# Kernel optimization log

Hardware: AMD Instinct MI355X
Metric: run time of the kernel (lower is better)

The kernel has to match this reference:

```python
import jax, jax.numpy as jnp
import numpy as np
import math

B = 16
IMG_H = IMG_W = 1024.0
FEAT_SIZES = [256, 128, 64, 32, 16]
A = 3
NUMS = [A * s * s for s in FEAT_SIZES]   # anchors per FPN level
TOTAL = sum(NUMS)                        # 261888
PRE_NMS_TOP_N = 1000
POST_NMS_TOP_N = 1000
NMS_THRESH = 0.7
SCORE_THRESH = 0.0
MIN_SIZE = 1e-3
BBOX_XFORM_CLIP = math.log(1000.0 / 16.0)
LEVELS = jnp.asarray(np.concatenate([np.full(n, i, dtype=np.int64) for i, n in enumerate(NUMS)]))


def setup_inputs() -> dict:
    key = jax.random.key(0)
    k1, k2, k3 = jax.random.split(key, 3)
    objectness = jax.random.normal(k1, (B, TOTAL), dtype=jnp.float32)
    deltas = jax.random.normal(k2, (B, TOTAL, 4), dtype=jnp.float32) * 0.2
    u = jax.random.uniform(k3, (TOTAL, 4), dtype=jnp.float32)
    ctr = u[:, :2] * jnp.array([IMG_W, IMG_H], dtype=jnp.float32)
    wh = u[:, 2:] * 192.0 + 16.0
    anchors = jnp.concatenate([ctr - 0.5 * wh, ctr + 0.5 * wh], axis=-1)
    return {"objectness": objectness, "deltas": deltas, "anchors": anchors}


def _decode(deltas, anchors):
    # BoxCoder with weights (1,1,1,1); deltas [B,T,4], anchors [T,4] (broadcast)
    w = anchors[:, 2] - anchors[:, 0]
    h = anchors[:, 3] - anchors[:, 1]
    cx = anchors[:, 0] + 0.5 * w
    cy = anchors[:, 1] + 0.5 * h
    dx, dy = deltas[..., 0], deltas[..., 1]
    dw = jnp.minimum(deltas[..., 2], BBOX_XFORM_CLIP)
    dh = jnp.minimum(deltas[..., 3], BBOX_XFORM_CLIP)
    pcx = dx * w + cx
    pcy = dy * h + cy
    pw = jnp.exp(dw) * w
    ph = jnp.exp(dh) * h
    return jnp.stack([pcx - 0.5 * pw, pcy - 0.5 * ph, pcx + 0.5 * pw, pcy + 0.5 * ph], axis=-1)


def _iou_one_vs_all(box, boxes):
    lt = jnp.maximum(box[:2], boxes[:, :2])
    rb = jnp.minimum(box[2:], boxes[:, 2:])
    wh = jnp.clip(rb - lt, 0.0)
    inter = wh[:, 0] * wh[:, 1]
    a1 = (box[2] - box[0]) * (box[3] - box[1])
    a2 = (boxes[:, 2] - boxes[:, 0]) * (boxes[:, 3] - boxes[:, 1])
    return inter / (a1 + a2 - inter)


def _nms_image(boxes, scores, lvl):
    # clip_boxes_to_image
    x = jnp.clip(boxes[:, 0::2], 0.0, IMG_W)
    y = jnp.clip(boxes[:, 1::2], 0.0, IMG_H)
    boxes = jnp.stack([x[:, 0], y[:, 0], x[:, 1], y[:, 1]], axis=-1)
    # remove_small_boxes + score_thresh, expressed as masking (fixed shapes)
    ws = boxes[:, 2] - boxes[:, 0]
    hs = boxes[:, 3] - boxes[:, 1]
    valid = (ws >= MIN_SIZE) & (hs >= MIN_SIZE) & (scores >= SCORE_THRESH)
    s0 = jnp.where(valid, scores, -1.0)
    # batched_nms: offset boxes by level so cross-level boxes never overlap
    off = lvl.astype(boxes.dtype) * (jnp.max(boxes) + 1.0)
    boff = boxes + off[:, None]

    def step(s, _):
        j = jnp.argmax(s)
        sj = s[j]
        take = sj > 0.0  # sigmoid scores are in (0,1); -1 marks suppressed
        iou = _iou_one_vs_all(boff[j], boff)
        s = jnp.where(iou > NMS_THRESH, -1.0, s)
        s = s.at[j].set(-1.0)
        out_b = jnp.where(take, boxes[j], jnp.zeros(4, boxes.dtype))
        out_s = jnp.where(take, sj, jnp.zeros((), boxes.dtype))
        return s, (out_b, out_s)

    _, (ob, os) = jax.lax.scan(step, s0, None, length=POST_NMS_TOP_N)
    return ob, os  # [P,4], [P]


def reference(objectness, deltas, anchors):
    proposals = _decode(deltas, anchors)  # [B, TOTAL, 4]
    # per-level top-k (pre-NMS), offsets into the flat anchor axis
    idx_list, offset = [], 0
    for n in NUMS:
        k = min(PRE_NMS_TOP_N, n)
        _, idx = jax.lax.top_k(objectness[:, offset:offset + n], k)
        idx_list.append(idx + offset)
        offset += n
    top_idx = jnp.concatenate(idx_list, axis=1)  # [B, K], K = 4768
    scores = jax.nn.sigmoid(jnp.take_along_axis(objectness, top_idx, axis=1))
    boxes = jnp.take_along_axis(proposals, top_idx[..., None], axis=1)
    lvl = LEVELS[top_idx]
    ob, os = jax.vmap(_nms_image)(boxes, scores, lvl)  # [B,P,4], [B,P]
    return jnp.concatenate([ob, os[..., None]], axis=-1)  # [B, P, 5]
```

## Files before the change

kernel.cpp:

```cpp
#include <hip/hip_runtime.h>
#include <math.h>

#pragma clang fp contract(off)

#define NLVL 5
#define TOTALN 261888
#define NBATCH 16
#define CAP 1024
#define NPROB (NBATCH * NLVL)
#define POST_N 1000
#define NMS_TH 0.7f
#define MINSZ 1e-3f
#define IMGSZ 1024.0f
#define BBOX_CLIP 4.135166556742356f

#define M_TH 0x1.666667p-1

#define HBINS 2048
#define CCAP 4096
#define NBLK 65
#define LMS 17
#define NPAIR 136

__constant__ int c_loff[NLVL] = {0, 196608, 245760, 258048, 261120};
__constant__ int c_k[NLVL]    = {1000, 1000, 1000, 1000, 768};
__constant__ int c_nch[NLVL]  = {48, 12, 3, 1, 1};

__constant__ unsigned char c_pw[NPAIR] = {
    0, 1,1, 2,2,2, 3,3,3,3, 4,4,4,4,4, 5,5,5,5,5,5, 6,6,6,6,6,6,6,
    7,7,7,7,7,7,7,7, 8,8,8,8,8,8,8,8,8, 9,9,9,9,9,9,9,9,9,9,
    10,10,10,10,10,10,10,10,10,10,10, 11,11,11,11,11,11,11,11,11,11,11,11,
    12,12,12,12,12,12,12,12,12,12,12,12,12, 13,13,13,13,13,13,13,13,13,13,13,13,13,13,
    14,14,14,14,14,14,14,14,14,14,14,14,14,14,14,
    15,15,15,15,15,15,15,15,15,15,15,15,15,15,15,15};
__constant__ unsigned char c_pr[NPAIR] = {
    0, 0,1, 0,1,2, 0,1,2,3, 0,1,2,3,4, 0,1,2,3,4,5, 0,1,2,3,4,5,6,
    0,1,2,3,4,5,6,7, 0,1,2,3,4,5,6,7,8, 0,1,2,3,4,5,6,7,8,9,
    0,1,2,3,4,5,6,7,8,9,10, 0,1,2,3,4,5,6,7,8,9,10,11,
    0,1,2,3,4,5,6,7,8,9,10,11,12, 0,1,2,3,4,5,6,7,8,9,10,11,12,13,
    0,1,2,3,4,5,6,7,8,9,10,11,12,13,14,
    0,1,2,3,4,5,6,7,8,9,10,11,12,13,14,15};

__device__ __forceinline__ unsigned monokey(float f) {
    unsigned b = __float_as_uint(f);
    return (b & 0x80000000u) ? ~b : (b | 0x80000000u);
}

__device__ __forceinline__ void blk_span(int b, int& lvl, int& start, int& cnt) {
    if (b < 48)      { lvl = 0; start = b * 4096;                  cnt = 4096; }
    else if (b < 60) { lvl = 1; start = 196608 + (b - 48) * 4096;  cnt = 4096; }
    else if (b < 63) { lvl = 2; start = 245760 + (b - 60) * 4096;  cnt = 4096; }
    else if (b == 63){ lvl = 3; start = 258048;                    cnt = 3072; }
    else             { lvl = 4; start = 261120;                    cnt = 768;  }
}

__global__ __launch_bounds__(256) void hist_kernel(const float* __restrict__ obj_all,
                                                   unsigned* __restrict__ ghist,
                                                   int* __restrict__ donecnt,
                                                   unsigned* __restrict__ b1out) {
    __shared__ unsigned lh[HBINS];
    __shared__ int s_last;
    const int tid = threadIdx.x;
    const int img = blockIdx.x / NBLK, b = blockIdx.x - img * NBLK;
    int lvl, start, cnt;
    blk_span(b, lvl, start, cnt);
    const int p = img * NLVL + lvl;
    for (int i = tid; i < HBINS; i += 256) lh[i] = 0;
    __syncthreads();
    const float* o = obj_all + (size_t)img * TOTALN + start;
    for (int i = tid * 4; i < cnt; i += 1024) {
        float4 v = *(const float4*)(o + i);
        atomicAdd(&lh[monokey(v.x) >> 21], 1u);
        atomicAdd(&lh[monokey(v.y) >> 21], 1u);
        atomicAdd(&lh[monokey(v.z) >> 21], 1u);
        atomicAdd(&lh[monokey(v.w) >> 21], 1u);
    }
    __syncthreads();
    unsigned* gh = ghist + (size_t)p * HBINS;
    for (int i = tid; i < HBINS; i += 256) {
        unsigned v = lh[i];
        if (v) atomicAdd(&gh[i], v);
    }
    __syncthreads();
    if (tid == 0) s_last = (atomicAdd(&donecnt[p], 1) == c_nch[lvl] - 1) ? 1 : 0;
    __syncthreads();
    if (!s_last) return;

    for (int i = tid; i < HBINS; i += 256) lh[i] = atomicAdd(&gh[i], 0u);
    __syncthreads();
    const int k = c_k[lvl];
    for (int d = 1; d < HBINS; d <<= 1) {
        unsigned v[HBINS / 256];
#pragma unroll
        for (int r = 0; r < HBINS / 256; ++r) {
            int i = tid + r * 256;
            v[r] = lh[i] + ((i + d < HBINS) ? lh[i + d] : 0u);
        }
        __syncthreads();
#pragma unroll
        for (int r = 0; r < HBINS / 256; ++r) lh[tid + r * 256] = v[r];
        __syncthreads();
    }
#pragma unroll
    for (int r = 0; r < HBINS / 256; ++r) {
        int i = tid + r * 256;
        if (lh[i] >= (unsigned)k && (i == HBINS - 1 || lh[i + 1] < (unsigned)k))
            b1out[p] = (unsigned)i;
    }
}

__global__ __launch_bounds__(256) void compact_kernel(const float* __restrict__ obj_all,
                                                      const unsigned* __restrict__ b1in,
                                                      int* __restrict__ cnt,
                                                      unsigned long long* __restrict__ cand) {
    __shared__ unsigned long long lkey[4096];
    __shared__ int s_lc, s_base;
    const int tid = threadIdx.x;
    const int img = blockIdx.x / NBLK, b = blockIdx.x - img * NBLK;
    int lvl, start, nrem;
    blk_span(b, lvl, start, nrem);
    const int p = img * NLVL + lvl;
    const unsigned thr = b1in[p] << 21;
    const int local0 = start - c_loff[lvl];
    if (tid == 0) s_lc = 0;
    __syncthreads();
    const float* o = obj_all + (size_t)img * TOTALN + start;
    for (int i = tid * 4; i < nrem; i += 1024) {
        float4 v = *(const float4*)(o + i);
        unsigned kx = monokey(v.x), ky = monokey(v.y);
        unsigned kz = monokey(v.z), kw = monokey(v.w);
        if (kx >= thr) { int l = atomicAdd(&s_lc, 1);
            lkey[l] = (((unsigned long long)kx) << 32) | (unsigned)(~(unsigned)(local0 + i)); }
        if (ky >= thr) { int l = atomicAdd(&s_lc, 1);
            lkey[l] = (((unsigned long long)ky) << 32) | (unsigned)(~(unsigned)(local0 + i + 1)); }
        if (kz >= thr) { int l = atomicAdd(&s_lc, 1);
            lkey[l] = (((unsigned long long)kz) << 32) | (unsigned)(~(unsigned)(local0 + i + 2)); }
        if (kw >= thr) { int l = atomicAdd(&s_lc, 1);
            lkey[l] = (((unsigned long long)kw) << 32) | (unsigned)(~(unsigned)(local0 + i + 3)); }
    }
    __syncthreads();
    if (tid == 0) s_base = atomicAdd(&cnt[p], s_lc);
    __syncthreads();
    const int lc = s_lc, base = s_base;
    unsigned long long* cd = cand + (size_t)p * CCAP;
    for (int i = tid; i < lc; i += 256) {
        int pos = base + i;
        if (pos < CCAP) cd[pos] = lkey[i];
    }
}

__global__ __launch_bounds__(256) void rankdec_kernel(
    const unsigned long long* __restrict__ cand, const int* __restrict__ cnt,
    const float* __restrict__ obj_all, const float* __restrict__ deltas,
    const float* __restrict__ anchors,
    float4* __restrict__ cbox, float* __restrict__ csc, float* __restrict__ carea) {
    __shared__ unsigned long long skey[CCAP];
    const int p = blockIdx.x >> 4;
    const int blk = blockIdx.x & 15;
    const int tid = threadIdx.x;
    const int lvl = p % NLVL, img = p / NLVL, k = c_k[lvl];
    int n = cnt[p]; if (n > CCAP) n = CCAP;
    const int i0 = blk << 8;
    if (i0 >= n) return;
    const unsigned long long* cd = cand + (size_t)p * CCAP;
    const int n32 = (n + 31) & ~31;
    for (int i = tid; i < n32; i += 256) skey[i] = (i < n) ? cd[i] : 0ull;
    __syncthreads();
    const int i = i0 + tid;
    const unsigned long long my = (i < n) ? skey[i] : ~0ull;
    int r0 = 0, r1 = 0, r2 = 0, r3 = 0;
    for (int j = 0; j < n32; j += 32) {
        unsigned long long kk[32];
#pragma unroll
        for (int q = 0; q < 32; ++q) kk[q] = skey[j + q];
#pragma unroll
        for (int q = 0; q < 8; ++q) {
            r0 += (int)(kk[q] > my);
            r1 += (int)(kk[8 + q] > my);
            r2 += (int)(kk[16 + q] > my);
            r3 += (int)(kk[24 + q] > my);
        }
    }
    const int rank = (r0 + r1) + (r2 + r3);
    if (i < n && rank < k) {
        unsigned li = ~(unsigned)(my & 0xFFFFFFFFull);
        unsigned idx = (unsigned)c_loff[lvl] + li;
        float o = obj_all[(size_t)img * TOTALN + idx];
        const float4 dd = *(const float4*)(deltas + ((size_t)img * TOTALN + (size_t)idx) * 4);
        const float4 aa = *(const float4*)(anchors + (size_t)idx * 4);
        float a0 = aa.x, a1 = aa.y, a2 = aa.z, a3 = aa.w;
        float w = a2 - a0, h = a3 - a1;
        float cx = a0 + 0.5f * w, cy = a1 + 0.5f * h;
        float dx = dd.x, dy = dd.y;
        float dw = fminf(dd.z, BBOX_CLIP), dh = fminf(dd.w, BBOX_CLIP);
        float pcx = dx * w + cx, pcy = dy * h + cy;
        float pw = expf(dw) * w, ph = expf(dh) * h;
        float bx1 = pcx - 0.5f * pw, by1 = pcy - 0.5f * ph;
        float bx2 = pcx + 0.5f * pw, by2 = pcy + 0.5f * ph;
        float x1 = fminf(fmaxf(bx1, 0.f), IMGSZ);
        float y1 = fminf(fmaxf(by1, 0.f), IMGSZ);
        float x2 = fminf(fmaxf(bx2, 0.f), IMGSZ);
        float y2 = fminf(fmaxf(by2, 0.f), IMGSZ);
        float wsz = x2 - x1, hsz = y2 - y1;
        float scv = (wsz >= MINSZ && hsz >= MINSZ) ? 1.0f / (1.0f + expf(-o)) : 0.0f;
        cbox[(size_t)p * CAP + rank] = make_float4(x1, y1, x2, y2);
        csc[(size_t)p * CAP + rank] = scv;
        carea[(size_t)p * CAP + rank] = wsz * hsz;
    }
}

__global__ __launch_bounds__(256) void mask_kernel(const float4* __restrict__ cbox,
                                                   const float* __restrict__ carea,
                                                   unsigned long long* __restrict__ gmaskT,
                                                   unsigned long long* __restrict__ tdiag) {
    const int bid = blockIdx.x;
    const int p = bid / 34;
    const int wid = __builtin_amdgcn_readfirstlane(threadIdx.x >> 6);
    const int lane = threadIdx.x & 63;
    const int q = (bid - p * 34) * 4 + wid;
    const int w = c_pw[q], rc = c_pr[q];
    const int base = p * CAP;

    const float4 cb = cbox[base + (w << 6) + lane];
    const float car = carea[base + (w << 6) + lane];
    const float4* rowb = cbox + base + (rc << 6);
    const float* rowa = carea + base + (rc << 6);

    unsigned long long tbits = 0, myword = 0;
    const bool isdiag = (rc == w);
#pragma unroll 8
    for (int r = 0; r < 64; ++r) {
        const float4 rb = rowb[r];
        const float ar = rowa[r];
        float ltx = fmaxf(rb.x, cb.x), lty = fmaxf(rb.y, cb.y);
        float rbx = fminf(rb.z, cb.z), rby = fminf(rb.w, cb.w);
        float wx = fmaxf(rbx - ltx, 0.f), wy = fmaxf(rby - lty, 0.f);
        float inter = wx * wy;
        float un = (ar + car) - inter;
        bool sup = (un > 0.f) && ((double)inter >= M_TH * (double)un);
        unsigned long long bits = __ballot(sup);
        if (isdiag) {
            bits &= (0xFFFFFFFFFFFFFFFEull << r);
            if (sup && lane > r) tbits |= (1ull << r);
        }
        myword = (lane == r) ? bits : myword;
    }
    gmaskT[((size_t)p << 14) + ((size_t)w << 10) + (rc << 6) + lane] = myword;
    if (isdiag) tdiag[((size_t)p << 10) + (w << 6) + lane] = tbits;
}

__global__ __launch_bounds__(1024) void scan_kernel(
    const unsigned long long* __restrict__ gmaskT,
    const unsigned long long* __restrict__ tdiag,
    const float4* __restrict__ cbox, const float* __restrict__ csc,
    float* __restrict__ svbox, float* __restrict__ svsc, int* __restrict__ svcnt) {
    __shared__ unsigned long long lm[CAP * LMS];
    __shared__ float ssc[CAP];
    __shared__ unsigned short survL[CAP];
    __shared__ int s_ns;
    const int p = blockIdx.x, tid = threadIdx.x;
    const int lvl = p % NLVL, k = c_k[lvl];
    const int base = p * CAP;

    {
        const ulonglong2* g2 = (const ulonglong2*)(gmaskT + ((size_t)p << 14));
#pragma unroll
        for (int c = 0; c < 8; ++c) {
            ulonglong2 v = g2[c * 1024 + tid];
            const int e = (c * 1024 + tid) << 1;
            const int w = e >> 10, row = e & 1023;
            lm[row * LMS + w] = v.x;
            lm[(row + 1) * LMS + w] = v.y;
        }
        ssc[tid] = (tid < k) ? csc[base + tid] : 0.f;
    }
    __syncthreads();

    if (tid < 64) {
        const int lane = tid;
        const unsigned long long* td = tdiag + ((size_t)p << 10);
        unsigned long long tg = td[lane];
        const unsigned long long mybit = 1ull << lane;
        const unsigned long long below = mybit - 1ull;
        int ns = 0;
        for (int g = 0; g < 16; ++g) {
            unsigned long long tgn = (g < 15) ? td[((g + 1) << 6) + lane] : 0ull;
            unsigned long long wv = __ballot(ssc[(g << 6) + lane] <= 0.f);
            unsigned long long a0 = 0, a1 = 0, a2 = 0, a3 = 0;
            int j = lane;
            for (; j + 192 < ns; j += 256) {
                int r0 = survL[j], r1 = survL[j + 64];
                int r2 = survL[j + 128], r3 = survL[j + 192];
                a0 |= lm[r0 * LMS + g];
                a1 |= lm[r1 * LMS + g];
                a2 |= lm[r2 * LMS + g];
                a3 |= lm[r3 * LMS + g];
            }
            for (; j < ns; j += 64) a0 |= lm[((int)survL[j]) * LMS + g];
            unsigned long long accw = (a0 | a1) | (a2 | a3);
#pragma unroll
            for (int d2 = 1; d2 < 64; d2 <<= 1)
                accw |= (unsigned long long)__shfl_xor((unsigned long long)accw, d2);

            const unsigned long long alive = ~(wv | accw);
            unsigned long long A = alive;
#pragma unroll 1
            for (int it = 0; it < 64; ++it) {
                bool kill = (tg & A) != 0ull;
                unsigned long long An = alive & ~__ballot(kill);
                if (An == A) break;
                A = An;
            }
            if (A & mybit)
                survL[ns + __popcll(A & below)] = (unsigned short)((g << 6) + lane);
            ns += __popcll(A);
            tg = tgn;
        }
        if (lane == 0) s_ns = ns;
    }
    __syncthreads();

    const int ns = s_ns;
    for (int s = tid; s < ns; s += 1024) {
        int r = survL[s];
        svsc[base + s] = ssc[r];
        *(float4*)(svbox + ((size_t)(base + s)) * 4) = cbox[base + r];
    }
    if (tid == 0) svcnt[p] = ns;
}

__global__ __launch_bounds__(256) void merge_kernel(
    const float* __restrict__ svbox, const float* __restrict__ svsc,
    const int* __restrict__ svcnt, float* __restrict__ out) {
    __shared__ float sls[NLVL][CAP];
    __shared__ int scnt[NLVL];
    const int img = blockIdx.x / NLVL, l = blockIdx.x % NLVL;
    const int tid = threadIdx.x;
    if (tid < NLVL) scnt[tid] = svcnt[img * NLVL + tid];
    __syncthreads();
    for (int m = 0; m < NLVL; ++m) {
        int c = scnt[m];
        for (int i = tid; i < c; i += 256) sls[m][i] = svsc[(img * NLVL + m) * CAP + i];
    }
    __syncthreads();
    const int c = scnt[l];
    for (int i = tid; i < c; i += 256) {
        const float s = sls[l][i];
        int pos = i;
#pragma unroll
        for (int m = 0; m < NLVL; ++m) {
            if (m == l) continue;
            const int n2 = scnt[m];
            int lo = 0;
#pragma unroll
            for (int st = 512; st > 0; st >>= 1) {
                const int idx = lo + st;
                const bool ok = (idx <= n2);
                const float v = sls[m][ok ? idx - 1 : 0];
                const bool ahead = (m < l) ? (v >= s) : (v > s);
                if (ok && ahead) lo = idx;
            }
            pos += lo;
        }
        if (pos < POST_N) {
            const int src = (img * NLVL + l) * CAP + i;
            float* o = out + ((size_t)img * POST_N + pos) * 5;
            o[0] = svbox[(size_t)src * 4 + 0];
            o[1] = svbox[(size_t)src * 4 + 1];
            o[2] = svbox[(size_t)src * 4 + 2];
            o[3] = svbox[(size_t)src * 4 + 3];
            o[4] = s;
        }
    }
}

extern "C" void kernel_launch(void* const* d_in, const int* in_sizes, int n_in,
                              void* d_out, int out_size, void* d_ws, size_t ws_size,
                              hipStream_t stream) {
    const float* obj     = (const float*)d_in[0];
    const float* deltas  = (const float*)d_in[1];
    const float* anchors = (const float*)d_in[2];
    float* out = (float*)d_out;

    char* w = (char*)d_ws;
    size_t off = 0;
    auto alloc = [&](size_t bytes) -> void* {
        void* pp = w + off;
        off += (bytes + 511) & ~(size_t)511;
        return pp;
    };
    size_t z0 = off;
    unsigned* ghist   = (unsigned*)alloc((size_t)NPROB * HBINS * 4);
    int*      donecnt = (int*)alloc((size_t)NPROB * 4);
    int*      ccnt    = (int*)alloc((size_t)NPROB * 4);
    size_t zspan = off - z0;
    unsigned* b1buf = (unsigned*)alloc((size_t)NPROB * 4);
    unsigned long long* cand = (unsigned long long*)alloc((size_t)NPROB * CCAP * 8);
    float4*   cbox  = (float4*)alloc((size_t)NPROB * CAP * 16);
    float*    csc   = (float*)alloc((size_t)NPROB * CAP * 4);
    float*    carea = (float*)alloc((size_t)NPROB * CAP * 4);
    unsigned long long* gmaskT = (unsigned long long*)alloc((size_t)NPROB * CAP * 16 * 8);
    unsigned long long* tdiag = (unsigned long long*)alloc((size_t)NPROB * CAP * 8);
    float* svbox = (float*)alloc((size_t)NPROB * CAP * 16);
    float* svsc  = (float*)alloc((size_t)NPROB * CAP * 4);
    int*   svcnt = (int*)alloc((size_t)NPROB * 4);
    if (off > ws_size) return;

    hipMemsetAsync(ghist, 0, zspan, stream);
    hipMemsetAsync(d_out, 0, (size_t)out_size * sizeof(float), stream);

    hist_kernel<<<NBATCH * NBLK, 256, 0, stream>>>(obj, ghist, donecnt, b1buf);
    compact_kernel<<<NBATCH * NBLK, 256, 0, stream>>>(obj, b1buf, ccnt, cand);
    rankdec_kernel<<<NPROB * 16, 256, 0, stream>>>(cand, ccnt, obj, deltas, anchors,
                                                   cbox, csc, carea);
    mask_kernel<<<NPROB * 34, 256, 0, stream>>>(cbox, carea, gmaskT, tdiag);
    scan_kernel<<<NPROB, 1024, 0, stream>>>(gmaskT, tdiag, cbox, csc, svbox, svsc, svcnt);
    merge_kernel<<<NPROB, 256, 0, stream>>>(svbox, svsc, svcnt, out);
}
```

Before: 140.6 us.

## Store NMS suppression masks column-wise and resolve kills via alive-word ANDs in registers

The mask kernel now stores, for each candidate, a per-lane bitmask of which earlier rows in a 64-row group suppress it, instead of ballot-transposed row words plus a separate diagonal array. The scan kernel drops the 136KB shared-memory staging of the full mask and the survivor-list gather. Each lane instead loads up to 16 mask words for its column from global memory and ANDs them with stored per-group alive words. This cuts shared memory so scan blocks shrink to 256 threads, and removes the survivor-indexed loop. The cost is serialized global loads per group inside a single-wavefront scan, plus heavy register use from the fully unrolled arrays.

```diff
diff --git a/kernel.cpp b/kernel.cpp
--- a/kernel.cpp
+++ b/kernel.cpp
@@ -19,7 +19,6 @@
 #define HBINS 2048
 #define CCAP 4096
 #define NBLK 65
-#define LMS 17
 #define NPAIR 136
 
 __constant__ int c_loff[NLVL] = {0, 196608, 245760, 258048, 261120};
@@ -211,8 +210,7 @@
 
 __global__ __launch_bounds__(256) void mask_kernel(const float4* __restrict__ cbox,
                                                    const float* __restrict__ carea,
-                                                   unsigned long long* __restrict__ gmaskT,
-                                                   unsigned long long* __restrict__ tdiag) {
+                                                   unsigned long long* __restrict__ gmaskS) {
     const int bid = blockIdx.x;
     const int p = bid / 34;
     const int wid = __builtin_amdgcn_readfirstlane(threadIdx.x >> 6);
@@ -226,8 +224,7 @@
     const float4* rowb = cbox + base + (rc << 6);
     const float* rowa = carea + base + (rc << 6);
 
-    unsigned long long tbits = 0, myword = 0;
-    const bool isdiag = (rc == w);
+    unsigned slo = 0, shi = 0;
 #pragma unroll 8
     for (int r = 0; r < 64; ++r) {
         const float4 rb = rowb[r];
@@ -238,75 +235,51 @@
         float inter = wx * wy;
         float un = (ar + car) - inter;
         bool sup = (un > 0.f) && ((double)inter >= M_TH * (double)un);
-        unsigned long long bits = __ballot(sup);
-        if (isdiag) {
-            bits &= (0xFFFFFFFFFFFFFFFEull << r);
-            if (sup && lane > r) tbits |= (1ull << r);
-        }
-        myword = (lane == r) ? bits : myword;
-    }
-    gmaskT[((size_t)p << 14) + ((size_t)w << 10) + (rc << 6) + lane] = myword;
-    if (isdiag) tdiag[((size_t)p << 10) + (w << 6) + lane] = tbits;
-}
-
-__global__ __launch_bounds__(1024) void scan_kernel(
-    const unsigned long long* __restrict__ gmaskT,
-    const unsigned long long* __restrict__ tdiag,
+        if (r < 32) slo |= sup ? (1u << r) : 0u;
+        else        shi |= sup ? (1u << (r - 32)) : 0u;
+    }
+    unsigned long long sbits = (((unsigned long long)shi) << 32) | slo;
+    if (rc == w) sbits &= ((1ull << lane) - 1ull);
+    gmaskS[(((size_t)(p * 16 + rc)) << 10) + (w << 6) + lane] = sbits;
+}
+
+__global__ __launch_bounds__(256) void scan_kernel(
+    const unsigned long long* __restrict__ gmaskS,
     const float4* __restrict__ cbox, const float* __restrict__ csc,
     float* __restrict__ svbox, float* __restrict__ svsc, int* __restrict__ svcnt) {
-    __shared__ unsigned long long lm[CAP * LMS];
     __shared__ float ssc[CAP];
     __shared__ unsigned short survL[CAP];
     __shared__ int s_ns;
     const int p = blockIdx.x, tid = threadIdx.x;
     const int lvl = p % NLVL, k = c_k[lvl];
     const int base = p * CAP;
-
-    {
-        const ulonglong2* g2 = (const ulonglong2*)(gmaskT + ((size_t)p << 14));
-#pragma unroll
-        for (int c = 0; c < 8; ++c) {
-            ulonglong2 v = g2[c * 1024 + tid];
-            const int e = (c * 1024 + tid) << 1;
-            const int w = e >> 10, row = e & 1023;
-            lm[row * LMS + w] = v.x;
-            lm[(row + 1) * LMS + w] = v.y;
-        }
-        ssc[tid] = (tid < k) ? csc[base + tid] : 0.f;
-    }
+    for (int i = tid; i < CAP; i += 256) ssc[i] = (i < k) ? csc[base + i] : 0.f;
     __syncthreads();
 
     if (tid < 64) {
         const int lane = tid;
-        const unsigned long long* td = tdiag + ((size_t)p << 10);
-        unsigned long long tg = td[lane];
         const unsigned long long mybit = 1ull << lane;
         const unsigned long long below = mybit - 1ull;
+        const unsigned long long* gS = gmaskS + ((size_t)p << 14);
+        unsigned long long aw[16];
         int ns = 0;
+#pragma unroll
         for (int g = 0; g < 16; ++g) {
-            unsigned long long tgn = (g < 15) ? td[((g + 1) << 6) + lane] : 0ull;
+            unsigned long long kk[16];
+#pragma unroll
+            for (int rc = 0; rc <= g; ++rc)
+                kk[rc] = gS[(((size_t)rc) << 10) + (g << 6) + lane];
             unsigned long long wv = __ballot(ssc[(g << 6) + lane] <= 0.f);
-            unsigned long long a0 = 0, a1 = 0, a2 = 0, a3 = 0;
-            int j = lane;
-            for (; j + 192 < ns; j += 256) {
-                int r0 = survL[j], r1 = survL[j + 64];
-                int r2 = survL[j + 128], r3 = survL[j + 192];
-                a0 |= lm[r0 * LMS + g];
-                a1 |= lm[r1 * LMS + g];
-                a2 |= lm[r2 * LMS + g];
-                a3 |= lm[r3 * LMS + g];
-            }
-            for (; j < ns; j += 64) a0 |= lm[((int)survL[j]) * LMS + g];
-            unsigned long long accw = (a0 | a1) | (a2 | a3);
-#pragma unroll
-            for (int d2 = 1; d2 < 64; d2 <<= 1)
-                accw |= (unsigned long long)__shfl_xor((unsigned long long)accw, d2);
-
-            const unsigned long long alive = ~(wv | accw);
+            unsigned long long killed = 0;
+#pragma unroll
+            for (int w2 = 0; w2 < g; ++w2) killed |= kk[w2] & aw[w2];
+            const unsigned long long kmask = __ballot(killed != 0ull);
+            const unsigned long long alive = ~(wv | kmask);
+            const unsigned long long dg = kk[g];
             unsigned long long A = alive;
 #pragma unroll 1
             for (int it = 0; it < 64; ++it) {
-                bool kill = (tg & A) != 0ull;
+                bool kill = (dg & A) != 0ull;
                 unsigned long long An = alive & ~__ballot(kill);
                 if (An == A) break;
                 A = An;
@@ -314,14 +287,14 @@
             if (A & mybit)
                 survL[ns + __popcll(A & below)] = (unsigned short)((g << 6) + lane);
             ns += __popcll(A);
-            tg = tgn;
+            aw[g] = A;
         }
         if (lane == 0) s_ns = ns;
     }
     __syncthreads();
 
     const int ns = s_ns;
-    for (int s = tid; s < ns; s += 1024) {
+    for (int s = tid; s < ns; s += 256) {
         int r = survL[s];
         svsc[base + s] = ssc[r];
         *(float4*)(svbox + ((size_t)(base + s)) * 4) = cbox[base + r];
@@ -399,8 +372,7 @@
     float4*   cbox  = (float4*)alloc((size_t)NPROB * CAP * 16);
     float*    csc   = (float*)alloc((size_t)NPROB * CAP * 4);
     float*    carea = (float*)alloc((size_t)NPROB * CAP * 4);
-    unsigned long long* gmaskT = (unsigned long long*)alloc((size_t)NPROB * CAP * 16 * 8);
-    unsigned long long* tdiag = (unsigned long long*)alloc((size_t)NPROB * CAP * 8);
+    unsigned long long* gmaskS = (unsigned long long*)alloc((size_t)NPROB * 16 * CAP * 8);
     float* svbox = (float*)alloc((size_t)NPROB * CAP * 16);
     float* svsc  = (float*)alloc((size_t)NPROB * CAP * 4);
     int*   svcnt = (int*)alloc((size_t)NPROB * 4);
@@ -413,7 +385,7 @@
     compact_kernel<<<NBATCH * NBLK, 256, 0, stream>>>(obj, b1buf, ccnt, cand);
     rankdec_kernel<<<NPROB * 16, 256, 0, stream>>>(cand, ccnt, obj, deltas, anchors,
                                                    cbox, csc, carea);
-    mask_kernel<<<NPROB * 34, 256, 0, stream>>>(cbox, carea, gmaskT, tdiag);
-    scan_kernel<<<NPROB, 1024, 0, stream>>>(gmaskT, tdiag, cbox, csc, svbox, svsc, svcnt);
+    mask_kernel<<<NPROB * 34, 256, 0, stream>>>(cbox, carea, gmaskS);
+    scan_kernel<<<NPROB, 256, 0, stream>>>(gmaskS, cbox, csc, svbox, svsc, svcnt);
     merge_kernel<<<NPROB, 256, 0, stream>>>(svbox, svsc, svcnt, out);
 }
```

Measured after the change: 138.6 us. About the same (-1.4%).
